# Optimization experiments

Hardware: AMD Instinct MI355X
Metric: run time of the kernel (lower is better)

The kernel has to match this reference:

```python
import jax, jax.numpy as jnp
import numpy as np

KERNEL_SIZE = 11
PAD = KERNEL_SIZE // 2
SIGMA = (KERNEL_SIZE - 1) * 2.0  # default sigma in the torch module


def _gaussian_kernel(ks, sigma):
    x = np.arange(ks, dtype=np.float32)
    g = np.exp(-(x - ks // 2) ** 2 / (2.0 * sigma ** 2))
    g = g / g.sum()
    k2d = np.outer(g, g).astype(np.float32)
    return jnp.asarray(k2d)[None, None]  # [1,1,ks,ks]


def setup_inputs() -> dict:
    key = jax.random.key(0)
    k1, k2 = jax.random.split(key)
    B, C, H, W = 16, 1, 1024, 1024
    img1 = jax.random.uniform(k1, (B, C, H, W), dtype=jnp.float32)
    img2 = jax.random.uniform(k2, (B, C, H, W), dtype=jnp.float32)
    kernel = _gaussian_kernel(KERNEL_SIZE, SIGMA)
    return {"img1": img1, "img2": img2, "kernel": kernel}


def _conv(x, kernel):
    # single-channel conv2d, 'same' padding (pad = k//2)
    return jax.lax.conv_general_dilated(
        x, kernel, window_strides=(1, 1),
        padding=[(PAD, PAD), (PAD, PAD)],
        dimension_numbers=("NCHW", "OIHW", "NCHW"))


def reference(img1, img2, kernel):
    val_range = (jnp.maximum(img1.max(), img2.max())
                 - jnp.minimum(img1.min(), img2.min()) + 1e-5)
    mu1 = _conv(img1, kernel)
    mu2 = _conv(img2, kernel)
    d1 = img1 - mu1
    d2 = img2 - mu2
    sigma1_sq = _conv(d1 * d1, kernel) + 1.0
    sigma2_sq = _conv(d2 * d2, kernel) + 1.0
    sigma12 = _conv(d1 * d2, kernel) + 1.0
    mu1_sq = mu1 * mu1 + 1.0
    mu2_sq = mu2 * mu2 + 1.0
    mu1mu2 = mu1 * mu2 + 1.0
    C1 = (0.01 * val_range) ** 2
    C2 = (0.03 * val_range) ** 2
    structure = (2.0 * sigma12 + C2) / (sigma1_sq + sigma2_sq + C2)
    brightness = ((2.0 * mu1mu2) ** 2 + C1) / ((mu1_sq + mu2_sq) ** 2 + C1)
    ssim_map = structure * brightness  # valid_mask=None -> all-ones mask
    return 1.0 - ssim_map.mean()
```

## Files before the change

### kernel.cpp

```cpp
#include <hip/hip_runtime.h>


#define IMG_H 1024
#define IMG_W 1024
#define USEC   44
#define NSTRIP 24
#define BAND   64
#define NBAND  16
#define NBATCH 16
#define NWAVES (NSTRIP * NBAND * NBATCH)
#define NBLK   (NWAVES / 4)

__device__ __forceinline__ unsigned fkey(float f) {
  unsigned b = __float_as_uint(f);
  return (b & 0x80000000u) ? ~b : (b | 0x80000000u);
}
__device__ __forceinline__ float funkey(unsigned k) {
  return (k & 0x80000000u) ? __uint_as_float(k & 0x7FFFFFFFu)
                           : __uint_as_float(~k);
}

__device__ __forceinline__ float xlane(float v, int addr) {
  return __int_as_float(__builtin_amdgcn_ds_bpermute(addr, __float_as_int(v)));
}

__global__ void ssim_init(unsigned* __restrict__ ws) {
  ws[0] = 0u;
  ws[1] = 0u;
  ws[2] = 0u;
  ws[3] = 0xFFFFFFFFu;
  ws[4] = 0u;
}

__global__ __launch_bounds__(256, 2)
void ssim_main(const float* __restrict__ img1, const float* __restrict__ img2,
               const float* __restrict__ kern, unsigned* __restrict__ ws) {
  __shared__ float redbuf[4][8];

  const int tid = threadIdx.x;
  const int lane = tid & 63;
  const int wv = tid >> 6;
  const int wid = blockIdx.x * 4 + wv;

  const int strip = wid % NSTRIP;
  const int rem = wid / NSTRIP;
  const int band = rem % NBAND;
  const int batch = rem / NBAND;

  const size_t boff = (size_t)batch * (IMG_H * IMG_W);
  const float* i1 = img1 + boff;
  const float* i2 = img2 + boff;

  float g[11];
  #pragma unroll
  for (int j = 0; j < 11; ++j) g[j] = kern[55 + j] * rsqrtf(kern[60]);

  const int col = strip * USEC + lane - 10;
  const bool cok = (col >= 0) && (col < IMG_W);
  const int cidx = min(max(col, 0), IMG_W - 1);
  const bool oma = (lane >= 10) && (lane < 54) && (col < IMG_W);
  const int r0 = band * BAND;
  const int a4 = lane * 4;

  float w1[11] = {}, w2[11] = {};
  float m1w[11] = {}, m2w[11] = {};
  float p11[11] = {}, p22[11] = {}, p12[11] = {};

  float acc0 = 0.f, aC1 = 0.f, aC2 = 0.f;
  float vmin = 1e30f, vmax = -1e30f;

  float nv1, nv2;
  {
    int rin = r0 - 10;
    if ((unsigned)rin < IMG_H) {
      nv1 = i1[(size_t)rin * IMG_W + cidx];
      nv2 = i2[(size_t)rin * IMG_W + cidx];
    } else { nv1 = 0.f; nv2 = 0.f; }
  }

  #pragma unroll 1
  for (int m = 0; m < 8; ++m) {
    #pragma unroll
    for (int c = 0; c < 11; ++c) {
      const int t = m * 11 + c;

      float v1 = cok ? nv1 : 0.f;
      float v2 = cok ? nv2 : 0.f;
      w1[c] = v1; w2[c] = v2;
      vmin = fminf(vmin, fminf(v1, v2));
      vmax = fmaxf(vmax, fmaxf(v1, v2));

      if (t < 83) {
        int rin = r0 - 9 + t;
        if ((unsigned)rin < IMG_H) {
          nv1 = i1[(size_t)rin * IMG_W + cidx];
          nv2 = i2[(size_t)rin * IMG_W + cidx];
        } else { nv1 = 0.f; nv2 = 0.f; }
      } else { nv1 = 0.f; nv2 = 0.f; }

      float V1 = 0.f, V2 = 0.f;
      #pragma unroll
      for (int j = 0; j < 11; ++j) {
        V1 = fmaf(g[j], w1[(c + 1 + j) % 11], V1);
        V2 = fmaf(g[j], w2[(c + 1 + j) % 11], V2);
      }

      float mu1 = g[5] * V1, mu2 = g[5] * V2;
      #pragma unroll
      for (int o = 1; o <= 5; ++o) {
        float l1 = xlane(V1, a4 - 4 * o);
        float r1 = xlane(V1, a4 + 4 * o);
        float l2 = xlane(V2, a4 - 4 * o);
        float r2 = xlane(V2, a4 + 4 * o);
        float sg = g[5 + o];
        mu1 = fmaf(sg, l1 + r1, mu1);
        mu2 = fmaf(sg, l2 + r2, mu2);
      }
      m1w[c] = mu1; m2w[c] = mu2;

      const bool drok = ((unsigned)(r0 - 15 + t) < IMG_H);
      float d1 = (drok && cok) ? (w1[(c + 6) % 11] - mu1) : 0.f;
      float d2 = (drok && cok) ? (w2[(c + 6) % 11] - mu2) : 0.f;

      float h11 = (g[5] * d1) * d1;
      float h22 = (g[5] * d2) * d2;
      float h12 = (g[5] * d1) * d2;
      #pragma unroll
      for (int o = 1; o <= 5; ++o) {
        float l1 = xlane(d1, a4 - 4 * o);
        float l2 = xlane(d2, a4 - 4 * o);
        float r1 = xlane(d1, a4 + 4 * o);
        float r2 = xlane(d2, a4 + 4 * o);
        float u = g[5 + o];
        h11 = fmaf(u, fmaf(l1, l1, r1 * r1), h11);
        h22 = fmaf(u, fmaf(l2, l2, r2 * r2), h22);
        h12 = fmaf(u, fmaf(l1, l2, r1 * r2), h12);
      }
      p11[c] = h11; p22[c] = h22; p12[c] = h12;

      if (t >= 20 && t < 84) {
        float s11 = 0.f, s22 = 0.f, s12 = 0.f;
        #pragma unroll
        for (int j = 0; j < 11; ++j) {
          float gj = g[j];
          s11 = fmaf(gj, p11[(c + 1 + j) % 11], s11);
          s22 = fmaf(gj, p22[(c + 1 + j) % 11], s22);
          s12 = fmaf(gj, p12[(c + 1 + j) % 11], s12);
        }
        float M1 = m1w[(c + 6) % 11], M2 = m2w[(c + 6) % 11];

        float s1 = s11 + 1.f;
        float s2 = s22 + 1.f;
        float sv = s12 + 1.f;
        float a = 2.f * sv;
        float b = s1 + s2;
        float rb = __builtin_amdgcn_rcpf(b);
        float S0 = a * rb;
        float Sp = (b - a) * rb * rb;
        float m12 = fmaf(M1, M2, 1.f);
        float nb = 2.f * m12;
        float N1 = nb * nb;
        float ms = fmaf(M1, M1, fmaf(M2, M2, 2.f));
        float Dv = ms * ms;
        float rD = __builtin_amdgcn_rcpf(Dv);
        float B0 = N1 * rD;
        float Bp = (Dv - N1) * rD * rD;
        float t0v = S0 * B0, t1v = S0 * Bp, t2v = B0 * Sp;
        acc0 += oma ? t0v : 0.f;
        aC1 += oma ? t1v : 0.f;
        aC2 += oma ? t2v : 0.f;
      }
    }
  }

  #pragma unroll
  for (int off = 32; off > 0; off >>= 1) {
    acc0 += __shfl_down(acc0, off);
    aC1 += __shfl_down(aC1, off);
    aC2 += __shfl_down(aC2, off);
    vmin = fminf(vmin, __shfl_down(vmin, off));
    vmax = fmaxf(vmax, __shfl_down(vmax, off));
  }
  if (lane == 0) {
    redbuf[wv][0] = acc0; redbuf[wv][1] = aC1; redbuf[wv][2] = aC2;
    redbuf[wv][3] = vmin; redbuf[wv][4] = vmax;
  }
  __syncthreads();
  if (tid == 0) {
    float t0 = 0.f, t1 = 0.f, t2 = 0.f, mn = 1e30f, mx = -1e30f;
    #pragma unroll
    for (int w2 = 0; w2 < 4; ++w2) {
      t0 += redbuf[w2][0]; t1 += redbuf[w2][1]; t2 += redbuf[w2][2];
      mn = fminf(mn, redbuf[w2][3]); mx = fmaxf(mx, redbuf[w2][4]);
    }
    float* wsF = (float*)ws;
    atomicAdd(&wsF[0], t0);
    atomicAdd(&wsF[1], t1);
    atomicAdd(&wsF[2], t2);
    atomicMin(&ws[3], fkey(mn));
    atomicMax(&ws[4], fkey(mx));
  }
}

__global__ void ssim_final(const unsigned* __restrict__ ws, float* __restrict__ out) {
  const float* wsF = (const float*)ws;
  float mn = funkey(ws[3]);
  float mx = funkey(ws[4]);
  float vr = mx - mn + 1e-5f;
  float c1 = 0.01f * vr; c1 *= c1;
  float c2 = 0.03f * vr; c2 *= c2;
  float mean = (wsF[0] + c1 * wsF[1] + c2 * wsF[2]) * (1.0f / 16777216.0f);
  out[0] = 1.f - mean;
}

extern "C" void kernel_launch(void* const* d_in, const int* in_sizes, int n_in,
                              void* d_out, int out_size, void* d_ws, size_t ws_size,
                              hipStream_t stream) {
  const float* img1 = (const float*)d_in[0];
  const float* img2 = (const float*)d_in[1];
  const float* kern = (const float*)d_in[2];
  unsigned* ws = (unsigned*)d_ws;
  float* out = (float*)d_out;
  (void)in_sizes; (void)n_in; (void)out_size; (void)ws_size;

  hipLaunchKernelGGL(ssim_init, dim3(1), dim3(1), 0, stream, ws);
  hipLaunchKernelGGL(ssim_main, dim3(NBLK), dim3(256), 0, stream,
                     img1, img2, kern, ws);
  hipLaunchKernelGGL(ssim_final, dim3(1), dim3(1), 0, stream, ws, out);
}
```

Before: 370.9 us.

## Process two columns per lane with fp16-packed cross-lane halo exchange

Each lane now handles two adjacent columns, so a wave covers 108 output columns instead of 44. The redundant halo loads and arithmetic per output shrink, and the number of strips drops from 24 to 10. Horizontal-pass intermediates are packed as half2 before ds_bpermute, which halves the permute count, and the row windows for mu and the product terms are also stored as packed fp16 to save registers. The separate final kernel is folded into the main kernel through a last-block-done atomic counter. The cost is fp16 rounding of intermediate convolution values, which may reduce accuracy of the SSIM result.

```diff
diff --git a/kernel.cpp b/kernel.cpp
--- a/kernel.cpp
+++ b/kernel.cpp
@@ -1,10 +1,11 @@
 #include <hip/hip_runtime.h>
+#include <hip/hip_fp16.h>
 
 
 #define IMG_H 1024
 #define IMG_W 1024
-#define USEC   44
-#define NSTRIP 24
+#define USEC   108
+#define NSTRIP 10
 #define BAND   64
 #define NBAND  16
 #define NBATCH 16
@@ -19,9 +20,17 @@
   return (k & 0x80000000u) ? __uint_as_float(k & 0x7FFFFFFFu)
                            : __uint_as_float(~k);
 }
-
-__device__ __forceinline__ float xlane(float v, int addr) {
-  return __int_as_float(__builtin_amdgcn_ds_bpermute(addr, __float_as_int(v)));
+__device__ __forceinline__ unsigned xlane_u(unsigned v, int addr) {
+  return (unsigned)__builtin_amdgcn_ds_bpermute(addr, (int)v);
+}
+__device__ __forceinline__ float lo2f(unsigned u) {
+  __half2 h = *(__half2*)&u; return __low2float(h);
+}
+__device__ __forceinline__ float hi2f(unsigned u) {
+  __half2 h = *(__half2*)&u; return __high2float(h);
+}
+__device__ __forceinline__ unsigned packh2(float a, float b) {
+  __half2 h = __floats2half2_rn(a, b); return *(unsigned*)&h;
 }
 
 __global__ void ssim_init(unsigned* __restrict__ ws) {
@@ -30,11 +39,13 @@
   ws[2] = 0u;
   ws[3] = 0xFFFFFFFFu;
   ws[4] = 0u;
+  ws[5] = 0u;
 }
 
 __global__ __launch_bounds__(256, 2)
 void ssim_main(const float* __restrict__ img1, const float* __restrict__ img2,
-               const float* __restrict__ kern, unsigned* __restrict__ ws) {
+               const float* __restrict__ kern, unsigned* __restrict__ ws,
+               float* __restrict__ out) {
   __shared__ float redbuf[4][8];
 
   const int tid = threadIdx.x;
@@ -55,28 +66,65 @@
   #pragma unroll
   for (int j = 0; j < 11; ++j) g[j] = kern[55 + j] * rsqrtf(kern[60]);
 
-  const int col = strip * USEC + lane - 10;
-  const bool cok = (col >= 0) && (col < IMG_W);
-  const int cidx = min(max(col, 0), IMG_W - 1);
-  const bool oma = (lane >= 10) && (lane < 54) && (col < IMG_W);
+  const int base = strip * USEC - 10;
+  const int c0 = base + 2 * lane;
+  const int c1v = c0 + 1;
+  const bool coka = ((unsigned)c0 < IMG_W);
+  const bool cokb = ((unsigned)c1v < IMG_W);
+  const int cia = min(max(c0, 0), IMG_W - 1);
+  const int cib = min(max(c1v, 0), IMG_W - 1);
+  const bool interior = (base >= 0) && (base + 128 <= IMG_W);
+  const bool omaa = (lane >= 5) && (lane <= 58) && coka;
+  const bool omab = (lane >= 5) && (lane <= 58) && cokb;
   const int r0 = band * BAND;
   const int a4 = lane * 4;
 
-  float w1[11] = {}, w2[11] = {};
-  float m1w[11] = {}, m2w[11] = {};
-  float p11[11] = {}, p22[11] = {}, p12[11] = {};
+  float w1a[11] = {}, w1b[11] = {}, w2a[11] = {}, w2b[11] = {};
+  unsigned m1w[11] = {}, m2w[11] = {};
+  unsigned p11w[11] = {}, p22w[11] = {}, p12w[11] = {};
 
   float acc0 = 0.f, aC1 = 0.f, aC2 = 0.f;
   float vmin = 1e30f, vmax = -1e30f;
 
-  float nv1, nv2;
-  {
-    int rin = r0 - 10;
+  auto LOADROW = [&](int rin, float2& o1, float2& o2) {
     if ((unsigned)rin < IMG_H) {
-      nv1 = i1[(size_t)rin * IMG_W + cidx];
-      nv2 = i2[(size_t)rin * IMG_W + cidx];
-    } else { nv1 = 0.f; nv2 = 0.f; }
-  }
+      const float* r1p = i1 + (size_t)rin * IMG_W;
+      const float* r2p = i2 + (size_t)rin * IMG_W;
+      if (interior) {
+        o1 = *(const float2*)(r1p + c0);
+        o2 = *(const float2*)(r2p + c0);
+      } else {
+        o1.x = r1p[cia]; o1.y = r1p[cib];
+        o2.x = r2p[cia]; o2.y = r2p[cib];
+      }
+    } else { o1.x = 0.f; o1.y = 0.f; o2.x = 0.f; o2.y = 0.f; }
+  };
+
+  auto COMB = [&](float s11, float s22, float s12v, float M1, float M2,
+                  bool ok, float& A0, float& A1, float& A2) {
+    float s1 = s11 + 1.f;
+    float s2 = s22 + 1.f;
+    float sv = s12v + 1.f;
+    float a = 2.f * sv;
+    float b = s1 + s2;
+    float rb = __builtin_amdgcn_rcpf(b);
+    float S0 = a * rb;
+    float Sp = (b - a) * rb * rb;
+    float m12 = fmaf(M1, M2, 1.f);
+    float nb = 2.f * m12;
+    float N1 = nb * nb;
+    float ms = fmaf(M1, M1, fmaf(M2, M2, 2.f));
+    float Dv = ms * ms;
+    float rD = __builtin_amdgcn_rcpf(Dv);
+    float B0 = N1 * rD;
+    float Bp = (Dv - N1) * rD * rD;
+    A0 += ok ? (S0 * B0) : 0.f;
+    A1 += ok ? (S0 * Bp) : 0.f;
+    A2 += ok ? (B0 * Sp) : 0.f;
+  };
+
+  float2 nv1, nv2;
+  LOADROW(r0 - 10, nv1, nv2);
 
   #pragma unroll 1
   for (int m = 0; m < 8; ++m) {
@@ -84,91 +132,125 @@
     for (int c = 0; c < 11; ++c) {
       const int t = m * 11 + c;
 
-      float v1 = cok ? nv1 : 0.f;
-      float v2 = cok ? nv2 : 0.f;
-      w1[c] = v1; w2[c] = v2;
-      vmin = fminf(vmin, fminf(v1, v2));
-      vmax = fmaxf(vmax, fmaxf(v1, v2));
-
-      if (t < 83) {
-        int rin = r0 - 9 + t;
-        if ((unsigned)rin < IMG_H) {
-          nv1 = i1[(size_t)rin * IMG_W + cidx];
-          nv2 = i2[(size_t)rin * IMG_W + cidx];
-        } else { nv1 = 0.f; nv2 = 0.f; }
-      } else { nv1 = 0.f; nv2 = 0.f; }
-
-      float V1 = 0.f, V2 = 0.f;
+      float v1a = coka ? nv1.x : 0.f;
+      float v1b = cokb ? nv1.y : 0.f;
+      float v2a = coka ? nv2.x : 0.f;
+      float v2b = cokb ? nv2.y : 0.f;
+      w1a[c] = v1a; w1b[c] = v1b; w2a[c] = v2a; w2b[c] = v2b;
+      vmin = fminf(vmin, fminf(fminf(v1a, v1b), fminf(v2a, v2b)));
+      vmax = fmaxf(vmax, fmaxf(fmaxf(v1a, v1b), fmaxf(v2a, v2b)));
+
+      if (t < 83) { LOADROW(r0 - 9 + t, nv1, nv2); }
+      else { nv1.x = 0.f; nv1.y = 0.f; nv2.x = 0.f; nv2.y = 0.f; }
+
+      float V1a = 0.f, V1b = 0.f, V2a = 0.f, V2b = 0.f;
       #pragma unroll
       for (int j = 0; j < 11; ++j) {
-        V1 = fmaf(g[j], w1[(c + 1 + j) % 11], V1);
-        V2 = fmaf(g[j], w2[(c + 1 + j) % 11], V2);
-      }
-
-      float mu1 = g[5] * V1, mu2 = g[5] * V2;
+        const int ix = (c + 1 + j) % 11;
+        const float gj = g[j];
+        V1a = fmaf(gj, w1a[ix], V1a); V1b = fmaf(gj, w1b[ix], V1b);
+        V2a = fmaf(gj, w2a[ix], V2a); V2b = fmaf(gj, w2b[ix], V2b);
+      }
+
+      const unsigned W1 = packh2(V1a, V1b), W2 = packh2(V2a, V2b);
+      const unsigned vl1_1 = xlane_u(W1, a4 - 4),  vl2_1 = xlane_u(W1, a4 - 8);
+      const unsigned vl3_1 = xlane_u(W1, a4 - 12), vr1_1 = xlane_u(W1, a4 + 4);
+      const unsigned vr2_1 = xlane_u(W1, a4 + 8),  vr3_1 = xlane_u(W1, a4 + 12);
+      const unsigned vl1_2 = xlane_u(W2, a4 - 4),  vl2_2 = xlane_u(W2, a4 - 8);
+      const unsigned vl3_2 = xlane_u(W2, a4 - 12), vr1_2 = xlane_u(W2, a4 + 4);
+      const unsigned vr2_2 = xlane_u(W2, a4 + 8),  vr3_2 = xlane_u(W2, a4 + 12);
+      float tp1[12], tp2[12];
+      tp1[0] = hi2f(vl3_1); tp1[1] = lo2f(vl2_1); tp1[2] = hi2f(vl2_1);
+      tp1[3] = lo2f(vl1_1); tp1[4] = hi2f(vl1_1);
+      tp1[5] = V1a; tp1[6] = V1b;
+      tp1[7] = lo2f(vr1_1); tp1[8] = hi2f(vr1_1);
+      tp1[9] = lo2f(vr2_1); tp1[10] = hi2f(vr2_1); tp1[11] = lo2f(vr3_1);
+      tp2[0] = hi2f(vl3_2); tp2[1] = lo2f(vl2_2); tp2[2] = hi2f(vl2_2);
+      tp2[3] = lo2f(vl1_2); tp2[4] = hi2f(vl1_2);
+      tp2[5] = V2a; tp2[6] = V2b;
+      tp2[7] = lo2f(vr1_2); tp2[8] = hi2f(vr1_2);
+      tp2[9] = lo2f(vr2_2); tp2[10] = hi2f(vr2_2); tp2[11] = lo2f(vr3_2);
+
+      float mu1a = g[5] * tp1[5], mu1b = g[5] * tp1[6];
+      float mu2a = g[5] * tp2[5], mu2b = g[5] * tp2[6];
       #pragma unroll
-      for (int o = 1; o <= 5; ++o) {
-        float l1 = xlane(V1, a4 - 4 * o);
-        float r1 = xlane(V1, a4 + 4 * o);
-        float l2 = xlane(V2, a4 - 4 * o);
-        float r2 = xlane(V2, a4 + 4 * o);
-        float sg = g[5 + o];
-        mu1 = fmaf(sg, l1 + r1, mu1);
-        mu2 = fmaf(sg, l2 + r2, mu2);
-      }
-      m1w[c] = mu1; m2w[c] = mu2;
+      for (int k = 1; k <= 5; ++k) {
+        const float gk = g[5 + k];
+        mu1a = fmaf(gk, tp1[5 - k] + tp1[5 + k], mu1a);
+        mu1b = fmaf(gk, tp1[6 - k] + tp1[6 + k], mu1b);
+        mu2a = fmaf(gk, tp2[5 - k] + tp2[5 + k], mu2a);
+        mu2b = fmaf(gk, tp2[6 - k] + tp2[6 + k], mu2b);
+      }
+      m1w[c] = packh2(mu1a, mu1b);
+      m2w[c] = packh2(mu2a, mu2b);
 
       const bool drok = ((unsigned)(r0 - 15 + t) < IMG_H);
-      float d1 = (drok && cok) ? (w1[(c + 6) % 11] - mu1) : 0.f;
-      float d2 = (drok && cok) ? (w2[(c + 6) % 11] - mu2) : 0.f;
-
-      float h11 = (g[5] * d1) * d1;
-      float h22 = (g[5] * d2) * d2;
-      float h12 = (g[5] * d1) * d2;
+      const int i6 = (c + 6) % 11;
+      float d1a = (drok && coka) ? (w1a[i6] - mu1a) : 0.f;
+      float d1b = (drok && cokb) ? (w1b[i6] - mu1b) : 0.f;
+      float d2a = (drok && coka) ? (w2a[i6] - mu2a) : 0.f;
+      float d2b = (drok && cokb) ? (w2b[i6] - mu2b) : 0.f;
+
+      const unsigned D1 = packh2(d1a, d1b), D2 = packh2(d2a, d2b);
+      const unsigned dl1_1 = xlane_u(D1, a4 - 4),  dl2_1 = xlane_u(D1, a4 - 8);
+      const unsigned dl3_1 = xlane_u(D1, a4 - 12), dr1_1 = xlane_u(D1, a4 + 4);
+      const unsigned dr2_1 = xlane_u(D1, a4 + 8),  dr3_1 = xlane_u(D1, a4 + 12);
+      const unsigned dl1_2 = xlane_u(D2, a4 - 4),  dl2_2 = xlane_u(D2, a4 - 8);
+      const unsigned dl3_2 = xlane_u(D2, a4 - 12), dr1_2 = xlane_u(D2, a4 + 4);
+      const unsigned dr2_2 = xlane_u(D2, a4 + 8),  dr3_2 = xlane_u(D2, a4 + 12);
+      float dp1[12], dp2[12];
+      dp1[0] = hi2f(dl3_1); dp1[1] = lo2f(dl2_1); dp1[2] = hi2f(dl2_1);
+      dp1[3] = lo2f(dl1_1); dp1[4] = hi2f(dl1_1);
+      dp1[5] = d1a; dp1[6] = d1b;
+      dp1[7] = lo2f(dr1_1); dp1[8] = hi2f(dr1_1);
+      dp1[9] = lo2f(dr2_1); dp1[10] = hi2f(dr2_1); dp1[11] = lo2f(dr3_1);
+      dp2[0] = hi2f(dl3_2); dp2[1] = lo2f(dl2_2); dp2[2] = hi2f(dl2_2);
+      dp2[3] = lo2f(dl1_2); dp2[4] = hi2f(dl1_2);
+      dp2[5] = d2a; dp2[6] = d2b;
+      dp2[7] = lo2f(dr1_2); dp2[8] = hi2f(dr1_2);
+      dp2[9] = lo2f(dr2_2); dp2[10] = hi2f(dr2_2); dp2[11] = lo2f(dr3_2);
+
+      float q11[12], q22[12], q12[12];
       #pragma unroll
-      for (int o = 1; o <= 5; ++o) {
-        float l1 = xlane(d1, a4 - 4 * o);
-        float l2 = xlane(d2, a4 - 4 * o);
-        float r1 = xlane(d1, a4 + 4 * o);
-        float r2 = xlane(d2, a4 + 4 * o);
-        float u = g[5 + o];
-        h11 = fmaf(u, fmaf(l1, l1, r1 * r1), h11);
-        h22 = fmaf(u, fmaf(l2, l2, r2 * r2), h22);
-        h12 = fmaf(u, fmaf(l1, l2, r1 * r2), h12);
-      }
-      p11[c] = h11; p22[c] = h22; p12[c] = h12;
+      for (int r = 0; r < 12; ++r) {
+        q11[r] = dp1[r] * dp1[r];
+        q22[r] = dp2[r] * dp2[r];
+        q12[r] = dp1[r] * dp2[r];
+      }
+      float h11a = g[5] * q11[5], h11b = g[5] * q11[6];
+      float h22a = g[5] * q22[5], h22b = g[5] * q22[6];
+      float h12a = g[5] * q12[5], h12b = g[5] * q12[6];
+      #pragma unroll
+      for (int k = 1; k <= 5; ++k) {
+        const float gk = g[5 + k];
+        h11a = fmaf(gk, q11[5 - k] + q11[5 + k], h11a);
+        h11b = fmaf(gk, q11[6 - k] + q11[6 + k], h11b);
+        h22a = fmaf(gk, q22[5 - k] + q22[5 + k], h22a);
+        h22b = fmaf(gk, q22[6 - k] + q22[6 + k], h22b);
+        h12a = fmaf(gk, q12[5 - k] + q12[5 + k], h12a);
+        h12b = fmaf(gk, q12[6 - k] + q12[6 + k], h12b);
+      }
+      p11w[c] = packh2(h11a, h11b);
+      p22w[c] = packh2(h22a, h22b);
+      p12w[c] = packh2(h12a, h12b);
 
       if (t >= 20 && t < 84) {
-        float s11 = 0.f, s22 = 0.f, s12 = 0.f;
+        float s11a = 0.f, s11b = 0.f, s22a = 0.f, s22b = 0.f;
+        float s12a = 0.f, s12b = 0.f;
         #pragma unroll
         for (int j = 0; j < 11; ++j) {
-          float gj = g[j];
-          s11 = fmaf(gj, p11[(c + 1 + j) % 11], s11);
-          s22 = fmaf(gj, p22[(c + 1 + j) % 11], s22);
-          s12 = fmaf(gj, p12[(c + 1 + j) % 11], s12);
+          const int ix = (c + 1 + j) % 11;
+          const float gj = g[j];
+          s11a = fmaf(gj, lo2f(p11w[ix]), s11a);
+          s11b = fmaf(gj, hi2f(p11w[ix]), s11b);
+          s22a = fmaf(gj, lo2f(p22w[ix]), s22a);
+          s22b = fmaf(gj, hi2f(p22w[ix]), s22b);
+          s12a = fmaf(gj, lo2f(p12w[ix]), s12a);
+          s12b = fmaf(gj, hi2f(p12w[ix]), s12b);
         }
-        float M1 = m1w[(c + 6) % 11], M2 = m2w[(c + 6) % 11];
-
-        float s1 = s11 + 1.f;
-        float s2 = s22 + 1.f;
-        float sv = s12 + 1.f;
-        float a = 2.f * sv;
-        float b = s1 + s2;
-        float rb = __builtin_amdgcn_rcpf(b);
-        float S0 = a * rb;
-        float Sp = (b - a) * rb * rb;
-        float m12 = fmaf(M1, M2, 1.f);
-        float nb = 2.f * m12;
-        float N1 = nb * nb;
-        float ms = fmaf(M1, M1, fmaf(M2, M2, 2.f));
-        float Dv = ms * ms;
-        float rD = __builtin_amdgcn_rcpf(Dv);
-        float B0 = N1 * rD;
-        float Bp = (Dv - N1) * rD * rD;
-        float t0v = S0 * B0, t1v = S0 * Bp, t2v = B0 * Sp;
-        acc0 += oma ? t0v : 0.f;
-        aC1 += oma ? t1v : 0.f;
-        aC2 += oma ? t2v : 0.f;
+        const unsigned mw1 = m1w[i6], mw2 = m2w[i6];
+        COMB(s11a, s22a, s12a, lo2f(mw1), lo2f(mw2), omaa, acc0, aC1, aC2);
+        COMB(s11b, s22b, s12b, hi2f(mw1), hi2f(mw2), omab, acc0, aC1, aC2);
       }
     }
   }
@@ -199,18 +281,22 @@
     atomicAdd(&wsF[2], t2);
     atomicMin(&ws[3], fkey(mn));
     atomicMax(&ws[4], fkey(mx));
+
+    __threadfence();
+    unsigned done = atomicAdd(&ws[5], 1u);
+    if (done == gridDim.x - 1) {
+      float s0 = atomicAdd(&wsF[0], 0.f);
+      float sc1 = atomicAdd(&wsF[1], 0.f);
+      float sc2 = atomicAdd(&wsF[2], 0.f);
+      unsigned mnk = atomicMin(&ws[3], 0xFFFFFFFFu);
+      unsigned mxk = atomicMax(&ws[4], 0u);
+      float vr = funkey(mxk) - funkey(mnk) + 1e-5f;
+      float c1 = 0.01f * vr; c1 *= c1;
+      float c2 = 0.03f * vr; c2 *= c2;
+      float mean = (s0 + c1 * sc1 + c2 * sc2) * (1.0f / 16777216.0f);
+      out[0] = 1.f - mean;
+    }
   }
-}
-
-__global__ void ssim_final(const unsigned* __restrict__ ws, float* __restrict__ out) {
-  const float* wsF = (const float*)ws;
-  float mn = funkey(ws[3]);
-  float mx = funkey(ws[4]);
-  float vr = mx - mn + 1e-5f;
-  float c1 = 0.01f * vr; c1 *= c1;
-  float c2 = 0.03f * vr; c2 *= c2;
-  float mean = (wsF[0] + c1 * wsF[1] + c2 * wsF[2]) * (1.0f / 16777216.0f);
-  out[0] = 1.f - mean;
 }
 
 extern "C" void kernel_launch(void* const* d_in, const int* in_sizes, int n_in,
@@ -225,6 +311,5 @@
 
   hipLaunchKernelGGL(ssim_init, dim3(1), dim3(1), 0, stream, ws);
   hipLaunchKernelGGL(ssim_main, dim3(NBLK), dim3(256), 0, stream,
-                     img1, img2, kern, ws);
-  hipLaunchKernelGGL(ssim_final, dim3(1), dim3(1), 0, stream, ws, out);
-}
+                     img1, img2, kern, ws, out);
+}
```

Measured after the change: 467.2 us. 26.0% more time.
